# Kernel tuning notes

Hardware: AMD Instinct MI355X
Metric: run time of the kernel (lower is better)

The kernel has to match this reference:

```python
import jax, jax.numpy as jnp
import numpy as np

DIM = 512
NUM_HEADS = 8
NUM_BLOCKS = 16
# NOTE: original code computes head_dim from FULL dim (before the reduce layer),
# so scale = (dim // num_heads) ** -0.5 = 64 ** -0.5, even though the actual
# per-head dim after reduce is 32. We preserve this quirk faithfully.
SCALE = (DIM // NUM_HEADS) ** -0.5


def setup_inputs() -> dict:
    key = jax.random.key(0)
    ks = jax.random.split(key, 5)
    B, N = 4, 4096
    C = DIM // 2
    x = jax.random.normal(ks[0], (B, N, DIM), dtype=jnp.float32)
    reduce_w = jax.random.normal(ks[1], (DIM, C), dtype=jnp.float32) * (DIM ** -0.5)
    qkv_w = jax.random.normal(ks[2], (C, 3 * C), dtype=jnp.float32) * (C ** -0.5)
    proj_w = jax.random.normal(ks[3], (C, DIM), dtype=jnp.float32) * (C ** -0.5)
    proj_b = jnp.zeros((DIM,), dtype=jnp.float32)
    return {"x": x, "reduce_w": reduce_w, "qkv_w": qkv_w,
            "proj_w": proj_w, "proj_b": proj_b}


def reference(x, reduce_w, qkv_w, proj_w, proj_b):
    B, N, _ = x.shape
    xr = x @ reduce_w                      # [B, N, C]  (C = dim/2)
    C = xr.shape[-1]
    H = NUM_HEADS
    d = C // H
    qkv = (xr @ qkv_w).reshape(B, N, 3, H, d).transpose(2, 0, 3, 1, 4)  # [3,B,H,N,d]
    q, k, v = qkv[0], qkv[1], qkv[2]
    bs = N // NUM_BLOCKS                   # block (chunk) size
    # block-diagonal local attention: reshape seq into independent blocks
    qb = q.reshape(B, H, NUM_BLOCKS, bs, d)
    kb = k.reshape(B, H, NUM_BLOCKS, bs, d)
    vb = v.reshape(B, H, NUM_BLOCKS, bs, d)
    attn = jnp.einsum('bhnqd,bhnkd->bhnqk', qb, kb) * SCALE
    attn = jax.nn.softmax(attn, axis=-1)
    ob = jnp.einsum('bhnqk,bhnkd->bhnqd', attn, vb)   # [B,H,Nb,bs,d]
    # torch: per-block transpose(1,2) then cat on dim=1 -> [B, N, H, d]
    o = ob.transpose(0, 2, 3, 1, 4).reshape(B, N, C)
    return o @ proj_w + proj_b
```

## Files before the change

### kernel.cpp

```cpp
#include <hip/hip_runtime.h>
#include <hip/hip_fp16.h>

typedef _Float16 half_t;
typedef _Float16 f16x8 __attribute__((ext_vector_type(8)));
typedef __fp16 fp16x2 __attribute__((ext_vector_type(2)));
typedef float f32x4 __attribute__((ext_vector_type(4)));

#define MFMA_F16(a, b, c) __builtin_amdgcn_mfma_f32_16x16x32_f16((a), (b), (c), 0, 0, 0)

static __device__ inline unsigned pkrtz(float a, float b) {
    union { fp16x2 h; unsigned u; } c;
    c.h = __builtin_amdgcn_cvt_pkrtz(a, b);
    return c.u;
}

__global__ __launch_bounds__(256) void prep(
    const float* __restrict__ qw, const float* __restrict__ rw,
    const float* __restrict__ pw, half_t* __restrict__ pw_t,
    half_t* __restrict__ Wt) {
    __shared__ __align__(16) char smem[24576];
    const int bid = blockIdx.x, tid = threadIdx.x;

    if (bid < 48) {
        char* As = smem;
        char* Bs = smem + 8192;
        const int M0 = (bid % 12) * 64, N0 = (bid / 12) * 128;
        const int lane = tid & 63, w = tid >> 6;
        const int l15 = lane & 15, l4 = lane >> 4;
        const int wrow = (w >> 1) * 32, wcol = (w & 1) * 64;
        const int pa = (l15 & 7) << 4;

        f32x4 acc[2][4];
#pragma unroll
        for (int i = 0; i < 2; ++i)
#pragma unroll
            for (int j = 0; j < 4; ++j) acc[i][j] = (f32x4){0.f, 0.f, 0.f, 0.f};

        for (int kc = 0; kc < 4; ++kc) {
            int c0 = kc * 64;
            __syncthreads();
#pragma unroll
            for (int i = 0; i < 2; ++i) {
                int j = tid + i * 256;
                int row = j >> 3, e8 = (j & 7) * 8;
                float s = (M0 + row) < 256 ? 0.18033688f : 1.f;
                f16x8 v;
#pragma unroll
                for (int e = 0; e < 8; ++e)
                    v[e] = (half_t)(qw[(size_t)(c0 + e8 + e) * 768 + M0 + row] * s);
                *(f16x8*)(As + row * 128 + ((e8 * 2) ^ ((row & 7) << 4))) = v;
            }
#pragma unroll
            for (int i = 0; i < 4; ++i) {
                int j = tid + i * 256;
                int row = j >> 3, e8 = (j & 7) * 8;
                const float* p = rw + (size_t)(N0 + row) * 256 + c0 + e8;
                float4 u0 = *(const float4*)p;
                float4 u1 = *(const float4*)(p + 4);
                f16x8 v;
                v[0] = (half_t)u0.x; v[1] = (half_t)u0.y;
                v[2] = (half_t)u0.z; v[3] = (half_t)u0.w;
                v[4] = (half_t)u1.x; v[5] = (half_t)u1.y;
                v[6] = (half_t)u1.z; v[7] = (half_t)u1.w;
                *(f16x8*)(Bs + row * 128 + ((e8 * 2) ^ ((row & 7) << 4))) = v;
            }
            __syncthreads();
#pragma unroll
            for (int ki = 0; ki < 2; ++ki) {
                f16x8 af[2], bf[4];
#pragma unroll
                for (int mi = 0; mi < 2; ++mi) {
                    int row = wrow + mi * 16 + l15;
                    af[mi] = *(const f16x8*)(As + row * 128 + (((ki * 4 + l4) << 4) ^ pa));
                }
#pragma unroll
                for (int nj = 0; nj < 4; ++nj) {
                    int row = wcol + nj * 16 + l15;
                    bf[nj] = *(const f16x8*)(Bs + row * 128 + (((ki * 4 + l4) << 4) ^ pa));
                }
#pragma unroll
                for (int mi = 0; mi < 2; ++mi)
#pragma unroll
                    for (int nj = 0; nj < 4; ++nj)
                        acc[mi][nj] = MFMA_F16(af[mi], bf[nj], acc[mi][nj]);
            }
        }
#pragma unroll
        for (int mi = 0; mi < 2; ++mi)
#pragma unroll
            for (int nj = 0; nj < 4; ++nj)
#pragma unroll
                for (int reg = 0; reg < 4; ++reg) {
                    int grow = M0 + wrow + mi * 16 + l4 * 4 + reg;
                    int gcol = N0 + wcol + nj * 16 + l15;
                    Wt[(size_t)grow * 512 + gcol] = (half_t)acc[mi][nj][reg];
                }
        return;
    }

    half_t* tile = (half_t*)smem;
    int t = bid - 48;
    int R0 = (t >> 3) * 64, C0 = (t & 7) * 64;
#pragma unroll
    for (int e = 0; e < 16; ++e) {
        int idx = tid + e * 256;
        int r = idx >> 6, c = idx & 63;
        tile[r * 72 + c] = (half_t)pw[(size_t)(R0 + r) * 512 + C0 + c];
    }
    __syncthreads();
#pragma unroll
    for (int e = 0; e < 16; ++e) {
        int idx = tid + e * 256;
        int c = idx >> 6, r = idx & 63;
        pw_t[(size_t)(C0 + c) * 256 + R0 + r] = tile[r * 72 + c];
    }
}

template <int EPI, bool AFP32, int NB, int K>
__global__ __launch_bounds__(256) void gemm_f16(
    const void* __restrict__ Aop, const half_t* __restrict__ Bt,
    void* __restrict__ Dst, const float* __restrict__ bias) {
    constexpr int nkt = K >> 6;
    constexpr int NBC = NB / 32;
    __shared__ __align__(16) char smem[8192 + NB * 128];
    char* As = smem;
    char* Bs = smem + 8192;

    const int tid = threadIdx.x;
    const int lane = tid & 63, w = tid >> 6;
    const int l15 = lane & 15, l4 = lane >> 4;
    const int wrow = (w >> 1) * 32, wcol = (w & 1) * (NB / 2);
    const int bm0 = blockIdx.x * 64;
    const int bn0 = blockIdx.y * NB;
    const int pa = (l15 & 7) << 4;

    f32x4 acc[2][NBC];
#pragma unroll
    for (int i = 0; i < 2; ++i)
#pragma unroll
        for (int j = 0; j < NBC; ++j) acc[i][j] = (f32x4){0.f, 0.f, 0.f, 0.f};

    f16x8 aReg[2], bReg[NBC];

    auto load_tile = [&](int kt) {
#pragma unroll
        for (int i = 0; i < 2; ++i) {
            int c = tid + i * 256;
            int row = c >> 3, k0 = (c & 7) * 8;
            int gk = kt * 64 + k0;
            if (AFP32) {
                const float* Af = (const float*)Aop + (size_t)(bm0 + row) * K + gk;
                float4 u0 = *(const float4*)Af;
                float4 u1 = *(const float4*)(Af + 4);
                f16x8 v;
                v[0] = (half_t)u0.x; v[1] = (half_t)u0.y;
                v[2] = (half_t)u0.z; v[3] = (half_t)u0.w;
                v[4] = (half_t)u1.x; v[5] = (half_t)u1.y;
                v[6] = (half_t)u1.z; v[7] = (half_t)u1.w;
                aReg[i] = v;
            } else {
                aReg[i] = *(const f16x8*)((const half_t*)Aop + (size_t)(bm0 + row) * K + gk);
            }
        }
#pragma unroll
        for (int i = 0; i < NBC; ++i) {
            int c = tid + i * 256;
            int row = c >> 3, k0 = (c & 7) * 8;
            bReg[i] = *(const f16x8*)(Bt + (size_t)(bn0 + row) * K + kt * 64 + k0);
        }
    };

    load_tile(0);
    for (int kt = 0; kt < nkt; ++kt) {
        __syncthreads();
#pragma unroll
        for (int i = 0; i < 2; ++i) {
            int c = tid + i * 256;
            int row = c >> 3, k0 = (c & 7) * 8;
            *(f16x8*)(As + row * 128 + ((k0 * 2) ^ ((row & 7) << 4))) = aReg[i];
        }
#pragma unroll
        for (int i = 0; i < NBC; ++i) {
            int c = tid + i * 256;
            int row = c >> 3, k0 = (c & 7) * 8;
            *(f16x8*)(Bs + row * 128 + ((k0 * 2) ^ ((row & 7) << 4))) = bReg[i];
        }
        __syncthreads();
        if (kt + 1 < nkt) load_tile(kt + 1);
#pragma unroll
        for (int ki = 0; ki < 2; ++ki) {
            f16x8 af[2], bf[NBC];
#pragma unroll
            for (int mi = 0; mi < 2; ++mi) {
                int row = wrow + mi * 16 + l15;
                af[mi] = *(const f16x8*)(As + row * 128 + (((ki * 4 + l4) << 4) ^ pa));
            }
#pragma unroll
            for (int nj = 0; nj < NBC; ++nj) {
                int row = wcol + nj * 16 + l15;
                bf[nj] = *(const f16x8*)(Bs + row * 128 + (((ki * 4 + l4) << 4) ^ pa));
            }
#pragma unroll
            for (int mi = 0; mi < 2; ++mi)
#pragma unroll
                for (int nj = 0; nj < NBC; ++nj)
                    acc[mi][nj] = MFMA_F16(af[mi], bf[nj], acc[mi][nj]);
        }
    }

#pragma unroll
    for (int mi = 0; mi < 2; ++mi) {
#pragma unroll
        for (int nj = 0; nj < NBC; ++nj) {
#pragma unroll
            for (int reg = 0; reg < 4; ++reg) {
                int grow = bm0 + wrow + mi * 16 + l4 * 4 + reg;
                int gcol = bn0 + wcol + nj * 16 + l15;
                float val = acc[mi][nj][reg];
                if (EPI == 1) {
                    int t = gcol >> 8, h = (gcol >> 5) & 7, dd = gcol & 31;
                    int b = grow >> 12, n = grow & 4095;
                    int blk = n >> 8, r = n & 255;
                    size_t idx = (size_t)t * 4194304 +
                                 (size_t)((((b << 3) + h) << 4) + blk) * 8192 +
                                 (size_t)r * 32 + dd;
                    ((half_t*)Dst)[idx] = (half_t)val;
                } else {
                    ((float*)Dst)[(size_t)grow * 512 + gcol] = val + bias[gcol];
                }
            }
        }
    }
}

__global__ __launch_bounds__(512, 4) void attn_f16(const half_t* __restrict__ qkv_ws,
                                                   half_t* __restrict__ o_ws) {
    __shared__ __align__(16) half_t VT[32 * 264];

    const int blkid = blockIdx.x;
    const int b = blkid >> 7, h = (blkid >> 4) & 7, blk = blkid & 15;
    const half_t* Q  = qkv_ws + (size_t)blkid * 8192;
    const half_t* Kp = qkv_ws + 4194304 + (size_t)blkid * 8192;
    const half_t* V  = qkv_ws + 8388608 + (size_t)blkid * 8192;

    const int tid = threadIdx.x, lane = tid & 63, w = tid >> 6;
    const int l15 = lane & 15, l4 = lane >> 4;
    const int qb = w * 32;

#pragma unroll
    for (int i = 0; i < 2; ++i) {
        int c = tid + i * 512;
        int key = c >> 2, k8 = (c & 3) * 8;
        f16x8 v = *(const f16x8*)(V + key * 32 + k8);
#pragma unroll
        for (int e = 0; e < 8; ++e) VT[(k8 + e) * 264 + key] = v[e];
    }

    f16x8 aq[2];
    aq[0] = *(const f16x8*)(Q + (qb + l15) * 32 + l4 * 8);
    aq[1] = *(const f16x8*)(Q + (qb + 16 + l15) * 32 + l4 * 8);

    __syncthreads();

    float s_run[2] = {0.f, 0.f};
    f32x4 acc_o[2][2];
#pragma unroll
    for (int qg = 0; qg < 2; ++qg)
#pragma unroll
        for (int fo = 0; fo < 2; ++fo) acc_o[qg][fo] = (f32x4){0.f, 0.f, 0.f, 0.f};
    const f32x4 zero4 = (f32x4){0.f, 0.f, 0.f, 0.f};

    for (int kt = 0; kt < 4; ++kt) {
        f16x8 ka[4];
#pragma unroll
        for (int t = 0; t < 4; ++t)
            ka[t] = *(const f16x8*)(Kp + (kt * 64 + t * 16 + l15) * 32 + l4 * 8);
        f16x8 bv[2][2];
#pragma unroll
        for (int c = 0; c < 2; ++c)
#pragma unroll
            for (int fo = 0; fo < 2; ++fo)
                bv[c][fo] = *(const f16x8*)&VT[(fo * 16 + l15) * 264 + kt * 64 + c * 32 + l4 * 8];

        f32x4 st[2][4];
        __builtin_amdgcn_s_setprio(1);
#pragma unroll
        for (int qg = 0; qg < 2; ++qg)
#pragma unroll
            for (int t = 0; t < 4; ++t) st[qg][t] = MFMA_F16(ka[t], aq[qg], zero4);
        __builtin_amdgcn_s_setprio(0);

#pragma unroll
        for (int qg = 0; qg < 2; ++qg) {
            float p[4][4];
            float ps = 0.f;
#pragma unroll
            for (int t = 0; t < 4; ++t)
#pragma unroll
                for (int r = 0; r < 4; ++r) {
                    float e = exp2f(st[qg][t][r]);
                    p[t][r] = e;
                    ps += e;
                }
            ps += __shfl_xor(ps, 16);
            ps += __shfl_xor(ps, 32);
            s_run[qg] += ps;

#pragma unroll
            for (int c = 0; c < 2; ++c) {
                unsigned pk0[2], pk1[2];
#pragma unroll
                for (int rp = 0; rp < 2; ++rp) {
                    pk0[rp] = pkrtz(p[2 * c][2 * rp], p[2 * c][2 * rp + 1]);
                    pk1[rp] = pkrtz(p[2 * c + 1][2 * rp], p[2 * c + 1][2 * rp + 1]);
                }
                union { unsigned u[4]; f16x8 v; } au;
#pragma unroll
                for (int j = 0; j < 4; ++j) {
                    int src = l15 + ((((l4 & 1) << 1) + (j >> 1)) << 4);
                    unsigned g0 = (unsigned)__shfl((int)pk0[j & 1], src);
                    unsigned g1 = (unsigned)__shfl((int)pk1[j & 1], src);
                    au.u[j] = (l4 < 2) ? g0 : g1;
                }
                __builtin_amdgcn_s_setprio(1);
#pragma unroll
                for (int fo = 0; fo < 2; ++fo)
                    acc_o[qg][fo] = MFMA_F16(au.v, bv[c][fo], acc_o[qg][fo]);
                __builtin_amdgcn_s_setprio(0);
            }
        }
    }

#pragma unroll
    for (int qg = 0; qg < 2; ++qg) {
        float inv = 1.f / s_run[qg];
        float sinv[4];
#pragma unroll
        for (int r = 0; r < 4; ++r) sinv[r] = __shfl(inv, (l4 << 2) | r);
#pragma unroll
        for (int fo = 0; fo < 2; ++fo)
#pragma unroll
            for (int r = 0; r < 4; ++r) {
                int grow = b * 4096 + blk * 256 + qb + qg * 16 + l4 * 4 + r;
                o_ws[(size_t)grow * 256 + h * 32 + fo * 16 + l15] =
                    (half_t)(acc_o[qg][fo][r] * sinv[r]);
            }
    }
}

extern "C" void kernel_launch(void* const* d_in, const int* in_sizes, int n_in,
                              void* d_out, int out_size, void* d_ws, size_t ws_size,
                              hipStream_t stream) {
    const float* x        = (const float*)d_in[0];
    const float* reduce_w = (const float*)d_in[1];
    const float* qkv_w    = (const float*)d_in[2];
    const float* proj_w   = (const float*)d_in[3];
    const float* proj_b   = (const float*)d_in[4];
    char* ws = (char*)d_ws;

    half_t* qkv_ws = (half_t*)ws;
    half_t* o_buf  = (half_t*)(ws + 25165824);
    half_t* pw_t   = (half_t*)(ws + 33554432);
    half_t* Wt     = (half_t*)(ws + 33816576);

    prep<<<80, 256, 0, stream>>>(qkv_w, reduce_w, proj_w, pw_t, Wt);
    gemm_f16<1, true, 192, 512><<<dim3(256, 4), 256, 0, stream>>>(x, Wt, qkv_ws, nullptr);
    attn_f16<<<512, 512, 0, stream>>>(qkv_ws, o_buf);
    gemm_f16<2, false, 256, 256><<<dim3(256, 2), 256, 0, stream>>>(o_buf, pw_t, d_out, proj_b);
}
```

Measured before the change: 65.83 us.

## Split GEMMs into specialized kernels reading B fragments directly from global memory

Replaces the templated GEMM with two specialized kernels. The QKV GEMM uses 512-thread blocks over 128-row tiles, stages only the fp32→fp16 converted activations in LDS (with a pre-swizzled global read), and loads weight fragments straight from global/L2 into registers. The projection GEMM drops LDS entirely and loads both operands directly as MFMA fragments. Both raise MFMA priority with s_setprio around the compute. This removes LDS staging and barriers for the small, cache-resident weights, at the cost of more global/L2 traffic per wave and higher register pressure.

Result: slower. 112.9 us (+71.5%).

```diff
diff --git a/kernel.cpp b/kernel.cpp
--- a/kernel.cpp
+++ b/kernel.cpp
@@ -116,118 +116,94 @@
     }
 }
 
-template <int EPI, bool AFP32, int NB, int K>
-__global__ __launch_bounds__(256) void gemm_f16(
-    const void* __restrict__ Aop, const half_t* __restrict__ Bt,
-    void* __restrict__ Dst, const float* __restrict__ bias) {
-    constexpr int nkt = K >> 6;
-    constexpr int NBC = NB / 32;
-    __shared__ __align__(16) char smem[8192 + NB * 128];
-    char* As = smem;
-    char* Bs = smem + 8192;
+__global__ __launch_bounds__(512) void gemm_qkv(
+    const float* __restrict__ X, const half_t* __restrict__ Wt,
+    half_t* __restrict__ Dst) {
+    __shared__ __align__(16) char As[16384];
 
     const int tid = threadIdx.x;
     const int lane = tid & 63, w = tid >> 6;
     const int l15 = lane & 15, l4 = lane >> 4;
-    const int wrow = (w >> 1) * 32, wcol = (w & 1) * (NB / 2);
-    const int bm0 = blockIdx.x * 64;
-    const int bn0 = blockIdx.y * NB;
+    const int wrow = (w >> 1) * 32, wcol = (w & 1) * 96;
+    const int bm0 = blockIdx.x * 128;
+    const int bn0 = blockIdx.y * 192;
     const int pa = (l15 & 7) << 4;
 
-    f32x4 acc[2][NBC];
+    f32x4 acc[2][6];
 #pragma unroll
     for (int i = 0; i < 2; ++i)
 #pragma unroll
-        for (int j = 0; j < NBC; ++j) acc[i][j] = (f32x4){0.f, 0.f, 0.f, 0.f};
-
-    f16x8 aReg[2], bReg[NBC];
-
-    auto load_tile = [&](int kt) {
+        for (int j = 0; j < 6; ++j) acc[i][j] = (f32x4){0.f, 0.f, 0.f, 0.f};
+
+    f16x8 aReg[2];
+    auto loadA = [&](int kt) {
 #pragma unroll
         for (int i = 0; i < 2; ++i) {
-            int c = tid + i * 256;
-            int row = c >> 3, k0 = (c & 7) * 8;
-            int gk = kt * 64 + k0;
-            if (AFP32) {
-                const float* Af = (const float*)Aop + (size_t)(bm0 + row) * K + gk;
-                float4 u0 = *(const float4*)Af;
-                float4 u1 = *(const float4*)(Af + 4);
-                f16x8 v;
-                v[0] = (half_t)u0.x; v[1] = (half_t)u0.y;
-                v[2] = (half_t)u0.z; v[3] = (half_t)u0.w;
-                v[4] = (half_t)u1.x; v[5] = (half_t)u1.y;
-                v[6] = (half_t)u1.z; v[7] = (half_t)u1.w;
-                aReg[i] = v;
-            } else {
-                aReg[i] = *(const f16x8*)((const half_t*)Aop + (size_t)(bm0 + row) * K + gk);
-            }
-        }
-#pragma unroll
-        for (int i = 0; i < NBC; ++i) {
-            int c = tid + i * 256;
-            int row = c >> 3, k0 = (c & 7) * 8;
-            bReg[i] = *(const f16x8*)(Bt + (size_t)(bn0 + row) * K + kt * 64 + k0);
+            int J = tid + i * 512;
+            int row = J >> 3, c = (J & 7) ^ (row & 7);
+            const float* p = X + (size_t)(bm0 + row) * 512 + kt * 64 + c * 8;
+            float4 u0 = *(const float4*)p;
+            float4 u1 = *(const float4*)(p + 4);
+            f16x8 v;
+            v[0] = (half_t)u0.x; v[1] = (half_t)u0.y;
+            v[2] = (half_t)u0.z; v[3] = (half_t)u0.w;
+            v[4] = (half_t)u1.x; v[5] = (half_t)u1.y;
+            v[6] = (half_t)u1.z; v[7] = (half_t)u1.w;
+            aReg[i] = v;
         }
     };
 
-    load_tile(0);
-    for (int kt = 0; kt < nkt; ++kt) {
+    loadA(0);
+    for (int kt = 0; kt < 8; ++kt) {
         __syncthreads();
 #pragma unroll
-        for (int i = 0; i < 2; ++i) {
-            int c = tid + i * 256;
-            int row = c >> 3, k0 = (c & 7) * 8;
-            *(f16x8*)(As + row * 128 + ((k0 * 2) ^ ((row & 7) << 4))) = aReg[i];
-        }
-#pragma unroll
-        for (int i = 0; i < NBC; ++i) {
-            int c = tid + i * 256;
-            int row = c >> 3, k0 = (c & 7) * 8;
-            *(f16x8*)(Bs + row * 128 + ((k0 * 2) ^ ((row & 7) << 4))) = bReg[i];
-        }
+        for (int i = 0; i < 2; ++i)
+            *(f16x8*)(As + (tid + i * 512) * 16) = aReg[i];
         __syncthreads();
-        if (kt + 1 < nkt) load_tile(kt + 1);
+        if (kt + 1 < 8) loadA(kt + 1);
+
+        f16x8 bf[2][6];
+#pragma unroll
+        for (int ki = 0; ki < 2; ++ki)
+#pragma unroll
+            for (int nj = 0; nj < 6; ++nj) {
+                int row = bn0 + wcol + nj * 16 + l15;
+                bf[ki][nj] = *(const f16x8*)(Wt + (size_t)row * 512 + kt * 64 + ki * 32 + l4 * 8);
+            }
 #pragma unroll
         for (int ki = 0; ki < 2; ++ki) {
-            f16x8 af[2], bf[NBC];
+            f16x8 af[2];
 #pragma unroll
             for (int mi = 0; mi < 2; ++mi) {
                 int row = wrow + mi * 16 + l15;
                 af[mi] = *(const f16x8*)(As + row * 128 + (((ki * 4 + l4) << 4) ^ pa));
             }
-#pragma unroll
-            for (int nj = 0; nj < NBC; ++nj) {
-                int row = wcol + nj * 16 + l15;
-                bf[nj] = *(const f16x8*)(Bs + row * 128 + (((ki * 4 + l4) << 4) ^ pa));
-            }
+            __builtin_amdgcn_s_setprio(1);
 #pragma unroll
             for (int mi = 0; mi < 2; ++mi)
 #pragma unroll
-                for (int nj = 0; nj < NBC; ++nj)
-                    acc[mi][nj] = MFMA_F16(af[mi], bf[nj], acc[mi][nj]);
+                for (int nj = 0; nj < 6; ++nj)
+                    acc[mi][nj] = MFMA_F16(af[mi], bf[ki][nj], acc[mi][nj]);
+            __builtin_amdgcn_s_setprio(0);
         }
     }
 
 #pragma unroll
     for (int mi = 0; mi < 2; ++mi) {
 #pragma unroll
-        for (int nj = 0; nj < NBC; ++nj) {
+        for (int nj = 0; nj < 6; ++nj) {
 #pragma unroll
             for (int reg = 0; reg < 4; ++reg) {
                 int grow = bm0 + wrow + mi * 16 + l4 * 4 + reg;
                 int gcol = bn0 + wcol + nj * 16 + l15;
                 float val = acc[mi][nj][reg];
-                if (EPI == 1) {
-                    int t = gcol >> 8, h = (gcol >> 5) & 7, dd = gcol & 31;
-                    int b = grow >> 12, n = grow & 4095;
-                    int blk = n >> 8, r = n & 255;
-                    size_t idx = (size_t)t * 4194304 +
-                                 (size_t)((((b << 3) + h) << 4) + blk) * 8192 +
-                                 (size_t)r * 32 + dd;
-                    ((half_t*)Dst)[idx] = (half_t)val;
-                } else {
-                    ((float*)Dst)[(size_t)grow * 512 + gcol] = val + bias[gcol];
-                }
+                int t = gcol >> 8, h = (gcol >> 5) & 7, dd = gcol & 31;
+                int b = grow >> 12, n = grow & 4095;
+                int blk = n >> 8, r = n & 255;
+                size_t idx = (size_t)t * 4194304 +
+                             (size_t)((((b << 3) + h) << 4) + blk) * 8192 +
+                             (size_t)r * 32 + dd;
+                Dst[idx] = (half_t)val;
             }
         }
     }
@@ -346,6 +322,58 @@
                     (half_t)(acc_o[qg][fo][r] * sinv[r]);
             }
     }
+}
+
+__global__ __launch_bounds__(256) void gemm_proj(
+    const half_t* __restrict__ A, const half_t* __restrict__ Bt,
+    float* __restrict__ Dst, const float* __restrict__ bias) {
+    const int tid = threadIdx.x;
+    const int lane = tid & 63, w = tid >> 6;
+    const int l15 = lane & 15, l4 = lane >> 4;
+    const int bm0 = blockIdx.x * 128;
+    const int bn0 = blockIdx.y * 128;
+    const int wrow = w * 32;
+
+    f32x4 acc[2][8];
+#pragma unroll
+    for (int i = 0; i < 2; ++i)
+#pragma unroll
+        for (int j = 0; j < 8; ++j) acc[i][j] = (f32x4){0.f, 0.f, 0.f, 0.f};
+
+    for (int kt = 0; kt < 4; ++kt) {
+#pragma unroll
+        for (int ki = 0; ki < 2; ++ki) {
+            f16x8 af[2], bf[8];
+#pragma unroll
+            for (int mi = 0; mi < 2; ++mi) {
+                int row = bm0 + wrow + mi * 16 + l15;
+                af[mi] = *(const f16x8*)(A + (size_t)row * 256 + kt * 64 + ki * 32 + l4 * 8);
+            }
+#pragma unroll
+            for (int nj = 0; nj < 8; ++nj) {
+                int row = bn0 + nj * 16 + l15;
+                bf[nj] = *(const f16x8*)(Bt + (size_t)row * 256 + kt * 64 + ki * 32 + l4 * 8);
+            }
+            __builtin_amdgcn_s_setprio(1);
+#pragma unroll
+            for (int mi = 0; mi < 2; ++mi)
+#pragma unroll
+                for (int nj = 0; nj < 8; ++nj)
+                    acc[mi][nj] = MFMA_F16(af[mi], bf[nj], acc[mi][nj]);
+            __builtin_amdgcn_s_setprio(0);
+        }
+    }
+
+#pragma unroll
+    for (int mi = 0; mi < 2; ++mi)
+#pragma unroll
+        for (int nj = 0; nj < 8; ++nj)
+#pragma unroll
+            for (int reg = 0; reg < 4; ++reg) {
+                int grow = bm0 + wrow + mi * 16 + l4 * 4 + reg;
+                int gcol = bn0 + nj * 16 + l15;
+                Dst[(size_t)grow * 512 + gcol] = acc[mi][nj][reg] + bias[gcol];
+            }
 }
 
 extern "C" void kernel_launch(void* const* d_in, const int* in_sizes, int n_in,
@@ -364,7 +392,7 @@
     half_t* Wt     = (half_t*)(ws + 33816576);
 
     prep<<<80, 256, 0, stream>>>(qkv_w, reduce_w, proj_w, pw_t, Wt);
-    gemm_f16<1, true, 192, 512><<<dim3(256, 4), 256, 0, stream>>>(x, Wt, qkv_ws, nullptr);
+    gemm_qkv<<<dim3(128, 4), 512, 0, stream>>>(x, Wt, qkv_ws);
     attn_f16<<<512, 512, 0, stream>>>(qkv_ws, o_buf);
-    gemm_f16<2, false, 256, 256><<<dim3(256, 2), 256, 0, stream>>>(o_buf, pw_t, d_out, proj_b);
-}
+    gemm_proj<<<dim3(128, 4), 256, 0, stream>>>(o_buf, pw_t, (float*)d_out, proj_b);
+}
```
